# Kernel optimization log

Hardware: AMD Instinct MI355X
Metric: run time of the kernel (lower is better)

## Reference

```python
import jax, jax.numpy as jnp
import numpy as np

N_EMBD = 2048
N_HEAD = 8          # config.n_head // 2
HEAD_DIM = 256      # n_embd // (n_head // 2)
HALF = HEAD_DIM // 2
LAMBDA_INIT = 0.8
RMS_EPS = 1.1920929e-07  # torch float32 finfo eps (F.rms_norm default)


def _rms_norm(x):
    # F.rms_norm with no weight: x / sqrt(mean(x^2) + eps)
    return x * jax.lax.rsqrt(jnp.mean(x * x, axis=-1, keepdims=True) + RMS_EPS)


def setup_inputs() -> dict:
    key = jax.random.key(0)
    ks = jax.random.split(key, 10)
    B, T, C = 2, 2048, N_EMBD
    x = jax.random.normal(ks[0], (B, T, C), dtype=jnp.float32)
    wq = jax.random.normal(ks[1], (C, C), dtype=jnp.float32) * 0.02
    wk = jax.random.normal(ks[2], (C, C), dtype=jnp.float32) * 0.02
    wv = jax.random.normal(ks[3], (C, C), dtype=jnp.float32) * 0.02
    wo = jax.random.normal(ks[4], (C, C), dtype=jnp.float32) * 0.02
    lq1 = jax.random.normal(ks[5], (HEAD_DIM,), dtype=jnp.float32) * 0.1
    lk1 = jax.random.normal(ks[6], (HEAD_DIM,), dtype=jnp.float32) * 0.1
    lq2 = jax.random.normal(ks[7], (HEAD_DIM,), dtype=jnp.float32) * 0.1
    lk2 = jax.random.normal(ks[8], (HEAD_DIM,), dtype=jnp.float32) * 0.1
    return {"x": x, "wq": wq, "wk": wk, "wv": wv, "wo": wo,
            "lq1": lq1, "lk1": lk1, "lq2": lq2, "lk2": lk2}


def _causal_attn(q, k, v, mask):
    # q,k: [B,H,T,half], v: [B,H,T,HEAD_DIM]
    scale = 1.0 / jnp.sqrt(jnp.asarray(q.shape[-1], q.dtype))
    scores = jnp.einsum('bhqd,bhkd->bhqk', q, k) * scale
    scores = jnp.where(mask, scores, -jnp.inf)
    attn = jax.nn.softmax(scores, axis=-1)
    return jnp.einsum('bhqk,bhkd->bhqd', attn, v)


def reference(x, wq, wk, wv, wo, lq1, lk1, lq2, lk2):
    B, T, C = x.shape
    lambda_1 = jnp.exp(jnp.sum(lq1 * lk1))
    lambda_2 = jnp.exp(jnp.sum(lq2 * lk2))
    lambda_full = lambda_1 - lambda_2 + LAMBDA_INIT

    q = (x @ wq.T).reshape(B, T, N_HEAD, 2, HALF).transpose(0, 2, 1, 3, 4)  # [B,H,T,2,half]
    k = (x @ wk.T).reshape(B, T, N_HEAD, 2, HALF).transpose(0, 2, 1, 3, 4)
    v = (x @ wv.T).reshape(B, T, N_HEAD, HEAD_DIM).transpose(0, 2, 1, 3)    # [B,H,T,hd]

    q1 = _rms_norm(q[..., 0, :]); q2 = _rms_norm(q[..., 1, :])
    k1 = _rms_norm(k[..., 0, :]); k2 = _rms_norm(k[..., 1, :])

    mask = jnp.tril(jnp.ones((T, T), dtype=bool))
    y1 = _causal_attn(q1, k1, v, mask)
    y2 = _causal_attn(q2, k2, v, mask)
    y = y1 - lambda_full * y2                                               # [B,H,T,hd]

    y = y.transpose(0, 2, 1, 3).reshape(B, T, C)
    return (y @ wo.T) * (1.0 - LAMBDA_INIT)
```

## Files before the change

### kernel.cpp

```cpp
#include <hip/hip_runtime.h>
#include <stdint.h>


typedef __bf16 bf16;
typedef bf16 bf16x8 __attribute__((ext_vector_type(8)));
typedef bf16 bf16x4 __attribute__((ext_vector_type(4)));
typedef bf16 bf16x2 __attribute__((ext_vector_type(2)));
typedef float f32x4 __attribute__((ext_vector_type(4)));

typedef void __attribute__((address_space(1)))* gas_t;
typedef void __attribute__((address_space(3)))* las_t;

__device__ __forceinline__ void gload16(const void* g, void* l) {
  __builtin_amdgcn_global_load_lds((gas_t)(uintptr_t)g, (las_t)(uint32_t)(uintptr_t)l, 16, 0, 0);
}

__device__ __forceinline__ f32x4 mfma16x16(bf16x8 a, bf16x8 b, f32x4 c) {
  return __builtin_amdgcn_mfma_f32_16x16x32_bf16(a, b, c, 0, 0, 0);
}

__global__ __launch_bounds__(256) void cast_f32_bf16(const float* __restrict__ in,
                                                     bf16* __restrict__ out, int n4) {
  int i = blockIdx.x * 256 + threadIdx.x;
  if (i >= n4) return;
  float4 v = ((const float4*)in)[i];
  bf16x4 o;
  o[0] = (bf16)v.x; o[1] = (bf16)v.y; o[2] = (bf16)v.z; o[3] = (bf16)v.w;
  ((bf16x4*)out)[i] = o;
}

__global__ __launch_bounds__(256) void cast4_w(const float* __restrict__ a, const float* __restrict__ b,
                                               const float* __restrict__ c, const float* __restrict__ d,
                                               bf16* __restrict__ oa, bf16* __restrict__ ob,
                                               bf16* __restrict__ oc, bf16* __restrict__ od) {
  int w = blockIdx.y;
  const float* in = (w == 0) ? a : (w == 1) ? b : (w == 2) ? c : d;
  bf16* out = (w == 0) ? oa : (w == 1) ? ob : (w == 2) ? oc : od;
  int i = blockIdx.x * 256 + threadIdx.x;
  float4 v = ((const float4*)in)[i];
  bf16x4 o;
  o[0] = (bf16)v.x; o[1] = (bf16)v.y; o[2] = (bf16)v.z; o[3] = (bf16)v.w;
  ((bf16x4*)out)[i] = o;
}

__global__ void lambda_kernel(const float* __restrict__ lq1, const float* __restrict__ lk1,
                              const float* __restrict__ lq2, const float* __restrict__ lk2,
                              float* __restrict__ out) {
  __shared__ float red[8];
  int tid = threadIdx.x;
  float a = lq1[tid] * lk1[tid];
  float b = lq2[tid] * lk2[tid];
#pragma unroll
  for (int m = 32; m >= 1; m >>= 1) {
    a += __shfl_xor(a, m, 64);
    b += __shfl_xor(b, m, 64);
  }
  if ((tid & 63) == 0) { red[tid >> 6] = a; red[4 + (tid >> 6)] = b; }
  __syncthreads();
  if (tid == 0) {
    float s1 = red[0] + red[1] + red[2] + red[3];
    float s2 = red[4] + red[5] + red[6] + red[7];
    out[0] = expf(s1) - expf(s2) + 0.8f;
  }
}

__global__ __launch_bounds__(512, 2) void gemm_qkv8(const bf16* __restrict__ A,
                                                    const bf16* __restrict__ Bq,
                                                    const bf16* __restrict__ Bk,
                                                    const bf16* __restrict__ Bv,
                                                    bf16* __restrict__ Cq, bf16* __restrict__ Ck,
                                                    bf16* __restrict__ Cv) {
  __shared__ char lds[98304];
  const int K = 2048, nt = 64;

  int p = blockIdx.y * gridDim.x + blockIdx.x;
  int lid = (p & 7) * 48 + (p >> 3);
  const int bm = (lid / 24) * 256;
  const int bnG = (lid % 24) * 256;
  const int z = bnG >> 11;
  const int bn = bnG & 2047;
  const bf16* B = (z == 0) ? Bq : ((z == 1) ? Bk : Bv);

  const int tid = threadIdx.x;
  const int wid = tid >> 6, lane = tid & 63;
  const int l15 = lane & 15, lhi = lane >> 4;
  const int wm = wid >> 2, wn = wid & 3;

  const bf16* aS0 = A + (size_t)(bm + wid * 16 + l15) * K + lhi * 8;
  const bf16* bS0 = B + (size_t)(bn + wid * 16 + l15) * K + lhi * 8;

  auto stA = [&](int t, int pb) {
    char* d = lds + pb * 32768 + wid * 1024;
    const bf16* s = aS0 + t * 32;
    gload16(s, d);
    gload16(s + (size_t)128 * K, d + 8192);
  };
  auto stB = [&](int t, int pb) {
    char* d = lds + pb * 32768 + 16384 + wid * 1024;
    const bf16* s = bS0 + t * 32;
    gload16(s, d);
    gload16(s + (size_t)128 * K, d + 8192);
  };

  const f32x4 fz = {0.f, 0.f, 0.f, 0.f};
  f32x4 acc[8][4];
#pragma unroll
  for (int m = 0; m < 8; ++m)
#pragma unroll
    for (int n = 0; n < 4; ++n) acc[m][n] = fz;

  stA(0, 0); stB(0, 0);
  stA(1, 1); stB(1, 1);
  asm volatile("s_waitcnt vmcnt(4)" ::: "memory");
  __builtin_amdgcn_s_barrier();

  int cur = 0;
  for (int t = 0; t < nt; ++t) {
    const char* ab = lds + cur * 32768;
    const char* bb = ab + 16384;
    int nx2 = cur + 2; if (nx2 >= 3) nx2 -= 3;
    bf16x8 a[8], b0, b1;

#pragma unroll
    for (int m = 0; m < 8; ++m) a[m] = *(const bf16x8*)(ab + (wm * 8 + m) * 1024 + lane * 16);
    b0 = *(const bf16x8*)(bb + (wn * 4 + 0) * 1024 + lane * 16);
    b1 = *(const bf16x8*)(bb + (wn * 4 + 1) * 1024 + lane * 16);
    if (t + 2 < nt) stA(t + 2, nx2);
    __builtin_amdgcn_s_barrier();
    __builtin_amdgcn_s_setprio(1);
#pragma unroll
    for (int m = 0; m < 8; ++m) {
      acc[m][0] = mfma16x16(a[m], b0, acc[m][0]);
      acc[m][1] = mfma16x16(a[m], b1, acc[m][1]);
    }
    __builtin_amdgcn_s_setprio(0);
    __builtin_amdgcn_s_barrier();

    b0 = *(const bf16x8*)(bb + (wn * 4 + 2) * 1024 + lane * 16);
    b1 = *(const bf16x8*)(bb + (wn * 4 + 3) * 1024 + lane * 16);
    if (t + 2 < nt) stB(t + 2, nx2);
    __builtin_amdgcn_s_barrier();
    __builtin_amdgcn_s_setprio(1);
#pragma unroll
    for (int m = 0; m < 8; ++m) {
      acc[m][2] = mfma16x16(a[m], b0, acc[m][2]);
      acc[m][3] = mfma16x16(a[m], b1, acc[m][3]);
    }
    __builtin_amdgcn_s_setprio(0);
    if (t + 2 < nt) {
      asm volatile("s_waitcnt vmcnt(4)" ::: "memory");
    } else {
      asm volatile("s_waitcnt vmcnt(0)" ::: "memory");
    }
    __builtin_amdgcn_s_barrier();

    cur = (cur == 2) ? 0 : cur + 1;
  }

  if (z == 2) {
#pragma unroll
    for (int m = 0; m < 8; ++m)
#pragma unroll
      for (int n = 0; n < 4; ++n)
#pragma unroll
        for (int r = 0; r < 4; ++r) {
          int row = bm + wm * 128 + m * 16 + lhi * 4 + r;
          int col = bn + wn * 64 + n * 16 + l15;
          int bb3 = row >> 11, tt = row & 2047;
          Cv[(size_t)bb3 * 2048 * 2048 + (size_t)col * 2048 + tt] = (bf16)acc[m][n][r];
        }
    return;
  }
  float* ldsf = (float*)lds;
#pragma unroll
  for (int m = 0; m < 8; ++m)
#pragma unroll
    for (int r = 0; r < 4; ++r) {
      float s = acc[m][0][r] * acc[m][0][r] + acc[m][1][r] * acc[m][1][r] +
                acc[m][2][r] * acc[m][2][r] + acc[m][3][r] * acc[m][3][r];
      s += __shfl_xor(s, 1, 64);
      s += __shfl_xor(s, 2, 64);
      s += __shfl_xor(s, 4, 64);
      s += __shfl_xor(s, 8, 64);
      if (l15 == 0) ldsf[(wm * 128 + m * 16 + lhi * 4 + r) * 4 + wn] = s;
    }
  __syncthreads();
  const float osc = (z == 0) ? 0.08838834764831845f : 1.0f;
  bf16* C = (z == 0) ? Cq : Ck;
#pragma unroll
  for (int m = 0; m < 8; ++m) {
#pragma unroll
    for (int r = 0; r < 4; ++r) {
      int rl = wm * 128 + m * 16 + lhi * 4 + r;
      float tot = ldsf[rl * 4 + (wn & 2)] + ldsf[rl * 4 + (wn & 2) + 1];
      float sc = rsqrtf(tot * (1.0f / 128.0f) + 1.1920929e-07f) * osc;
#pragma unroll
      for (int n = 0; n < 4; ++n) {
        int col = bn + wn * 64 + n * 16 + l15;
        C[(size_t)(bm + rl) * 2048 + col] = (bf16)(acc[m][n][r] * sc);
      }
    }
  }
}

__global__ __launch_bounds__(256, 2) void gemm_out(const bf16* __restrict__ A, const bf16* __restrict__ B,
                                                   float* __restrict__ Cf) {
  __shared__ char lds[73728];
  const int K = 2048, nt = 64;

  int p = blockIdx.y * gridDim.x + blockIdx.x;
  int lid = (p & 7) * 32 + (p >> 3);
  const int bm = (lid / 16) * 256;
  const int bn = (lid % 16) * 128;

  const int tid = threadIdx.x;
  const int wid = tid >> 6, lane = tid & 63;
  const int l15 = lane & 15, lhi = lane >> 4;
  const int wm = wid >> 1, wn = wid & 1;

  const bf16* aB = A + (size_t)(bm + l15) * K + lhi * 8;
  const bf16* bB = B + (size_t)(bn + l15) * K + lhi * 8;

  auto stage = [&](int t, int pb) {
    char* base = lds + pb * 24576;
    const int k0 = t * 32;
    gload16(aB + (size_t)((0 + wid) * 16) * K + k0, base + wid * 1024);
    gload16(aB + (size_t)((4 + wid) * 16) * K + k0, base + 4096 + wid * 1024);
    gload16(aB + (size_t)((8 + wid) * 16) * K + k0, base + 8192 + wid * 1024);
    gload16(aB + (size_t)((12 + wid) * 16) * K + k0, base + 12288 + wid * 1024);
    gload16(bB + (size_t)((0 + wid) * 16) * K + k0, base + 16384 + wid * 1024);
    gload16(bB + (size_t)((4 + wid) * 16) * K + k0, base + 20480 + wid * 1024);
  };

  const f32x4 fz = {0.f, 0.f, 0.f, 0.f};
  f32x4 acc[8][4];
#pragma unroll
  for (int m = 0; m < 8; ++m)
#pragma unroll
    for (int n = 0; n < 4; ++n) acc[m][n] = fz;

  stage(0, 0);
  stage(1, 1);
  asm volatile("s_waitcnt vmcnt(6)" ::: "memory");
  __builtin_amdgcn_s_barrier();

  for (int t = 0; t < nt; ++t) {
    const char* ab = lds + (t % 3) * 24576;
    if (t + 2 < nt) stage(t + 2, (t + 2) % 3);
    bf16x8 a[8], b[4];
#pragma unroll
    for (int m = 0; m < 8; ++m)
      a[m] = *(const bf16x8*)(ab + (wm * 8 + m) * 1024 + lane * 16);
#pragma unroll
    for (int n = 0; n < 4; ++n)
      b[n] = *(const bf16x8*)(ab + 16384 + (wn * 4 + n) * 1024 + lane * 16);
    __builtin_amdgcn_s_setprio(1);
#pragma unroll
    for (int m = 0; m < 8; ++m)
#pragma unroll
      for (int n = 0; n < 4; ++n) acc[m][n] = mfma16x16(a[m], b[n], acc[m][n]);
    __builtin_amdgcn_s_setprio(0);
    if (t + 2 < nt) {
      asm volatile("s_waitcnt vmcnt(6)" ::: "memory");
    } else {
      asm volatile("s_waitcnt vmcnt(0)" ::: "memory");
    }
    __builtin_amdgcn_s_barrier();
  }

#pragma unroll
  for (int m = 0; m < 8; ++m)
#pragma unroll
    for (int n = 0; n < 4; ++n)
#pragma unroll
      for (int r = 0; r < 4; ++r) {
        int row = bm + wm * 128 + m * 16 + lhi * 4 + r;
        int col = bn + wn * 64 + n * 16 + l15;
        Cf[(size_t)row * 2048 + col] = acc[m][n][r] * 0.2f;
      }
}

__global__ __launch_bounds__(256) void attn_kernel(const bf16* __restrict__ qb, const bf16* __restrict__ kb,
                                                   const bf16* __restrict__ vtb, bf16* __restrict__ yb,
                                                   const float* __restrict__ lamp) {
  __shared__ char lds[57344];
  const int tid = threadIdx.x;
  const int wid = tid >> 6, lane = tid & 63;
  const int l15 = lane & 15, lhi = lane >> 4;
  char* vtl = lds + 32768;
  char* p1l = lds + 49152 + wid * 2048;
  char* p2l = p1l + 1024;
  const int qt = 31 - blockIdx.y;
  const int bh = blockIdx.x;
  const int b = bh >> 3, h = bh & 7;
  const int qr0 = qt * 64 + wid * 16;
  const float lam = lamp[0];

  const bf16* qrow = qb + (size_t)(b * 2048 + qr0 + l15) * 2048 + h * 256 + lhi * 8;
  bf16x8 q1f[4], q2f[4];
#pragma unroll
  for (int s = 0; s < 4; ++s) {
    q1f[s] = *(const bf16x8*)(qrow + s * 32);
    q2f[s] = *(const bf16x8*)(qrow + 128 + s * 32);
  }

  const f32x4 fz = {0.f, 0.f, 0.f, 0.f};
  f32x4 y1[16], y2[16];
#pragma unroll
  for (int f = 0; f < 16; ++f) { y1[f] = fz; y2[f] = fz; }
  float l1[4] = {0.f, 0.f, 0.f, 0.f}, l2[4] = {0.f, 0.f, 0.f, 0.f};

  const int nkt = 2 * qt + 2;
  const bf16* kbase = kb + (size_t)(b * 2048) * 2048 + h * 256;
  const bf16* vbase = vtb + (size_t)b * 2048 * 2048 + (size_t)(h * 256) * 2048;

  auto stageK = [&](int kt2, int p) {
    const int t0 = kt2 * 32;
    char* kd = lds + p * 16384 + wid * 1024;
    const bf16* sp = kbase + (size_t)(t0 + l15) * 2048 + wid * 32 + lhi * 8;
    gload16(sp, kd);
    gload16(sp + 16 * 2048, kd + 4096);
    gload16(sp + 128, kd + 8192);
    gload16(sp + 16 * 2048 + 128, kd + 12288);
  };
  auto stageVT = [&](int kt2) {
    const int t0 = kt2 * 32;
    const bf16* vp = vbase + (size_t)(wid * 16 + l15) * 2048 + t0 + lhi * 8;
#pragma unroll
    for (int i = 0; i < 4; ++i)
      gload16(vp + (size_t)i * 64 * 2048, vtl + (i * 4 + wid) * 1024);
  };

  stageK(0, 0);
  stageVT(0);
  __syncthreads();

  for (int kt = 0; kt < nkt; ++kt) {
    const int cur = kt & 1;
    const int t0 = kt * 32;
    const bool active = (t0 <= qr0 + 15);
    if (active) {
      const char* kc = lds + cur * 16384;
      f32x4 s1g[2], s2g[2];
#pragma unroll
      for (int g = 0; g < 2; ++g) {
        f32x4 a1 = fz, a2 = fz;
#pragma unroll
        for (int s = 0; s < 4; ++s) {
          a1 = mfma16x16(q1f[s], *(const bf16x8*)(kc + ((g * 4 + s) * 64 + lane) * 16), a1);
          a2 = mfma16x16(q2f[s], *(const bf16x8*)(kc + 8192 + ((g * 4 + s) * 64 + lane) * 16), a2);
        }
        s1g[g] = a1;
        s2g[g] = a2;
      }
      if (t0 + 31 > qr0) {
#pragma unroll
        for (int g = 0; g < 2; ++g) {
          int col = t0 + g * 16 + l15;
#pragma unroll
          for (int r = 0; r < 4; ++r) {
            int row = qr0 + lhi * 4 + r;
            if (col > row) { s1g[g][r] = -1e30f; s2g[g][r] = -1e30f; }
          }
        }
      }
#pragma unroll
      for (int g = 0; g < 2; ++g) {
#pragma unroll
        for (int r = 0; r < 4; ++r) {
          float p1 = __expf(s1g[g][r] - 12.0f);
          float p2 = __expf(s2g[g][r] - 12.0f);
          l1[r] += p1;
          l2[r] += p2;
          int off = ((lhi * 4 + r) * 32 + g * 16 + l15) * 2;
          *(bf16*)(p1l + off) = (bf16)p1;
          *(bf16*)(p2l + off) = (bf16)p2;
        }
      }
    }
    __syncthreads();
    if (active) {
      bf16x8 pa1 = *(const bf16x8*)(p1l + (l15 * 32 + lhi * 8) * 2);
      bf16x8 pa2 = *(const bf16x8*)(p2l + (l15 * 32 + lhi * 8) * 2);
#pragma unroll
      for (int f = 0; f < 16; ++f) {
        bf16x8 vf = *(const bf16x8*)(vtl + (f * 64 + lane) * 16);
        y1[f] = mfma16x16(pa1, vf, y1[f]);
        y2[f] = mfma16x16(pa2, vf, y2[f]);
      }
    }
    __syncthreads();
    if (kt + 1 < nkt) {
      stageK(kt + 1, cur ^ 1);
      stageVT(kt + 1);
    }
  }

#pragma unroll
  for (int r = 0; r < 4; ++r) {
    float s1 = l1[r], s2 = l2[r];
#pragma unroll
    for (int m = 1; m <= 8; m <<= 1) {
      s1 += __shfl_xor(s1, m, 64);
      s2 += __shfl_xor(s2, m, 64);
    }
    float inv1 = 1.f / s1;
    float inv2 = lam / s2;
    int row = qr0 + lhi * 4 + r;
    bf16* orow = yb + (size_t)(b * 2048 + row) * 2048 + h * 256 + l15;
#pragma unroll
    for (int f = 0; f < 16; ++f) {
      float v = y1[f][r] * inv1 - y2[f][r] * inv2;
      orow[f * 16] = (bf16)v;
    }
  }
}

extern "C" void kernel_launch(void* const* d_in, const int* in_sizes, int n_in,
                              void* d_out, int out_size, void* d_ws, size_t ws_size,
                              hipStream_t stream) {
  const float* x = (const float*)d_in[0];
  const float* wq = (const float*)d_in[1];
  const float* wk = (const float*)d_in[2];
  const float* wv = (const float*)d_in[3];
  const float* wo = (const float*)d_in[4];
  const float* lq1 = (const float*)d_in[5];
  const float* lk1 = (const float*)d_in[6];
  const float* lq2 = (const float*)d_in[7];
  const float* lk2 = (const float*)d_in[8];
  float* out = (float*)d_out;
  char* ws = (char*)d_ws;

  if (ws_size < 117440516) return;

  bf16* xb = (bf16*)(ws + 0);
  bf16* wqb = (bf16*)(ws + 16777216);
  bf16* wkb = (bf16*)(ws + 25165824);
  bf16* wvb = (bf16*)(ws + 33554432);
  bf16* wob = (bf16*)(ws + 41943040);
  bf16* qbuf = (bf16*)(ws + 50331648);
  bf16* kbuf = (bf16*)(ws + 67108864);
  bf16* vtb = (bf16*)(ws + 83886080);
  bf16* ybuf = (bf16*)(ws + 100663296);
  float* lam = (float*)(ws + 117440512);

  cast_f32_bf16<<<8192, 256, 0, stream>>>(x, xb, 2097152);
  cast4_w<<<dim3(4096, 4), 256, 0, stream>>>(wq, wk, wv, wo, wqb, wkb, wvb, wob);
  lambda_kernel<<<1, 256, 0, stream>>>(lq1, lk1, lq2, lk2, lam);

  gemm_qkv8<<<dim3(24, 16), 512, 0, stream>>>(xb, wqb, wkb, wvb, qbuf, kbuf, vtb);

  attn_kernel<<<dim3(16, 32), 256, 0, stream>>>(qbuf, kbuf, vtb, ybuf, lam);

  gemm_out<<<dim3(8, 32), 256, 0, stream>>>(ybuf, wob, out);
}
```

Before: 357.8 us.

## Prefetch attention K/V tiles through registers and reorder the attention grid

Replaces the double-buffered global_load_lds staging of K and V^T with register prefetch. The next tile's global loads are issued at the top of each iteration and written to a single LDS buffer after a barrier. This shrinks LDS from 56KB to 40KB, which may raise occupancy. The barrier between the softmax-probability store and the PV MFMAs is removed, since each wave only reads its own P region. MFMA sections are wrapped in s_setprio, and the 2D grid is flattened so heavy query tiles are scheduled first. The cost is an extra barrier per iteration and more VGPRs for the prefetch registers.

```diff
diff --git a/kernel.cpp b/kernel.cpp
--- a/kernel.cpp
+++ b/kernel.cpp
@@ -283,15 +283,18 @@
 __global__ __launch_bounds__(256) void attn_kernel(const bf16* __restrict__ qb, const bf16* __restrict__ kb,
                                                    const bf16* __restrict__ vtb, bf16* __restrict__ yb,
                                                    const float* __restrict__ lamp) {
-  __shared__ char lds[57344];
+  __shared__ char lds[40960];
   const int tid = threadIdx.x;
   const int wid = tid >> 6, lane = tid & 63;
   const int l15 = lane & 15, lhi = lane >> 4;
-  char* vtl = lds + 32768;
-  char* p1l = lds + 49152 + wid * 2048;
+  char* ktl = lds;
+  char* vtl = lds + 16384;
+  char* p1l = lds + 32768 + wid * 2048;
   char* p2l = p1l + 1024;
-  const int qt = 31 - blockIdx.y;
-  const int bh = blockIdx.x;
+
+  const int p = blockIdx.x;
+  const int bh = p & 15;
+  const int qt = (p < 256) ? (31 - (p >> 4)) : ((p - 256) >> 4);
   const int b = bh >> 3, h = bh & 7;
   const int qr0 = qt * 64 + wid * 16;
   const float lam = lamp[0];
@@ -314,45 +317,60 @@
   const bf16* kbase = kb + (size_t)(b * 2048) * 2048 + h * 256;
   const bf16* vbase = vtb + (size_t)b * 2048 * 2048 + (size_t)(h * 256) * 2048;
 
-  auto stageK = [&](int kt2, int p) {
-    const int t0 = kt2 * 32;
-    char* kd = lds + p * 16384 + wid * 1024;
-    const bf16* sp = kbase + (size_t)(t0 + l15) * 2048 + wid * 32 + lhi * 8;
-    gload16(sp, kd);
-    gload16(sp + 16 * 2048, kd + 4096);
-    gload16(sp + 128, kd + 8192);
-    gload16(sp + 16 * 2048 + 128, kd + 12288);
+  const bf16* kS = kbase + (size_t)l15 * 2048 + wid * 32 + lhi * 8;
+  const bf16* vS = vbase + (size_t)(wid * 16 + l15) * 2048 + lhi * 8;
+
+  int4 rk0, rk1, rk2, rk3, rv0, rv1, rv2, rv3;
+  auto loadRegs = [&](int kt2) {
+    const bf16* ks = kS + (size_t)(kt2 * 32) * 2048;
+    rk0 = *(const int4*)(ks);
+    rk1 = *(const int4*)(ks + (size_t)16 * 2048);
+    rk2 = *(const int4*)(ks + 128);
+    rk3 = *(const int4*)(ks + (size_t)16 * 2048 + 128);
+    const bf16* vs = vS + kt2 * 32;
+    rv0 = *(const int4*)(vs);
+    rv1 = *(const int4*)(vs + (size_t)64 * 2048);
+    rv2 = *(const int4*)(vs + (size_t)128 * 2048);
+    rv3 = *(const int4*)(vs + (size_t)192 * 2048);
   };
-  auto stageVT = [&](int kt2) {
-    const int t0 = kt2 * 32;
-    const bf16* vp = vbase + (size_t)(wid * 16 + l15) * 2048 + t0 + lhi * 8;
-#pragma unroll
-    for (int i = 0; i < 4; ++i)
-      gload16(vp + (size_t)i * 64 * 2048, vtl + (i * 4 + wid) * 1024);
+  auto writeLds = [&]() {
+    char* kd = ktl + wid * 1024 + lane * 16;
+    *(int4*)(kd) = rk0;
+    *(int4*)(kd + 4096) = rk1;
+    *(int4*)(kd + 8192) = rk2;
+    *(int4*)(kd + 12288) = rk3;
+    char* vd = vtl + wid * 1024 + lane * 16;
+    *(int4*)(vd) = rv0;
+    *(int4*)(vd + 4096) = rv1;
+    *(int4*)(vd + 8192) = rv2;
+    *(int4*)(vd + 12288) = rv3;
   };
 
-  stageK(0, 0);
-  stageVT(0);
+  loadRegs(0);
+  writeLds();
   __syncthreads();
 
   for (int kt = 0; kt < nkt; ++kt) {
-    const int cur = kt & 1;
     const int t0 = kt * 32;
     const bool active = (t0 <= qr0 + 15);
+    const bool hasNext = (kt + 1 < nkt);
+    if (hasNext) loadRegs(kt + 1);
+
     if (active) {
-      const char* kc = lds + cur * 16384;
       f32x4 s1g[2], s2g[2];
+      __builtin_amdgcn_s_setprio(1);
 #pragma unroll
       for (int g = 0; g < 2; ++g) {
         f32x4 a1 = fz, a2 = fz;
 #pragma unroll
         for (int s = 0; s < 4; ++s) {
-          a1 = mfma16x16(q1f[s], *(const bf16x8*)(kc + ((g * 4 + s) * 64 + lane) * 16), a1);
-          a2 = mfma16x16(q2f[s], *(const bf16x8*)(kc + 8192 + ((g * 4 + s) * 64 + lane) * 16), a2);
+          a1 = mfma16x16(q1f[s], *(const bf16x8*)(ktl + ((g * 4 + s) * 64 + lane) * 16), a1);
+          a2 = mfma16x16(q2f[s], *(const bf16x8*)(ktl + 8192 + ((g * 4 + s) * 64 + lane) * 16), a2);
         }
         s1g[g] = a1;
         s2g[g] = a2;
       }
+      __builtin_amdgcn_s_setprio(0);
       if (t0 + 31 > qr0) {
 #pragma unroll
         for (int g = 0; g < 2; ++g) {
@@ -377,23 +395,20 @@
           *(bf16*)(p2l + off) = (bf16)p2;
         }
       }
-    }
-    __syncthreads();
-    if (active) {
       bf16x8 pa1 = *(const bf16x8*)(p1l + (l15 * 32 + lhi * 8) * 2);
       bf16x8 pa2 = *(const bf16x8*)(p2l + (l15 * 32 + lhi * 8) * 2);
+      __builtin_amdgcn_s_setprio(1);
 #pragma unroll
       for (int f = 0; f < 16; ++f) {
         bf16x8 vf = *(const bf16x8*)(vtl + (f * 64 + lane) * 16);
         y1[f] = mfma16x16(pa1, vf, y1[f]);
         y2[f] = mfma16x16(pa2, vf, y2[f]);
       }
+      __builtin_amdgcn_s_setprio(0);
     }
     __syncthreads();
-    if (kt + 1 < nkt) {
-      stageK(kt + 1, cur ^ 1);
-      stageVT(kt + 1);
-    }
+    if (hasNext) writeLds();
+    __syncthreads();
   }
 
 #pragma unroll
@@ -450,7 +465,7 @@
 
   gemm_qkv8<<<dim3(24, 16), 512, 0, stream>>>(xb, wqb, wkb, wvb, qbuf, kbuf, vtb);
 
-  attn_kernel<<<dim3(16, 32), 256, 0, stream>>>(qbuf, kbuf, vtb, ybuf, lam);
+  attn_kernel<<<512, 256, 0, stream>>>(qbuf, kbuf, vtb, ybuf, lam);
 
   gemm_out<<<dim3(8, 32), 256, 0, stream>>>(ybuf, wob, out);
 }
```

Measured after the change: 403.4 us. +12.7%, slower.

## Double-buffer V tiles and prefetch next K/V before compute in attention

Applied to the files above, without the earlier changes.

The attention kernel now double-buffers the transposed V tile alongside K. It issues the global-to-LDS loads for the next K/V tile at the start of each iteration rather than after compute, so the loads overlap with the QK and PV MFMA work. The barrier between the P stores and the PV stage is dropped because each wave only reads its own P scratch. MFMA sections are wrapped in s_setprio, and the 2D grid is flattened with an explicit block-to-(bh, q-tile) mapping. The cost is more LDS (72KB), which may limit how many blocks fit on a CU.

```diff
diff --git a/kernel.cpp b/kernel.cpp
--- a/kernel.cpp
+++ b/kernel.cpp
@@ -283,15 +283,16 @@
 __global__ __launch_bounds__(256) void attn_kernel(const bf16* __restrict__ qb, const bf16* __restrict__ kb,
                                                    const bf16* __restrict__ vtb, bf16* __restrict__ yb,
                                                    const float* __restrict__ lamp) {
-  __shared__ char lds[57344];
+  __shared__ char lds[73728];
   const int tid = threadIdx.x;
   const int wid = tid >> 6, lane = tid & 63;
   const int l15 = lane & 15, lhi = lane >> 4;
-  char* vtl = lds + 32768;
-  char* p1l = lds + 49152 + wid * 2048;
+  char* p1l = lds + 65536 + wid * 2048;
   char* p2l = p1l + 1024;
-  const int qt = 31 - blockIdx.y;
-  const int bh = blockIdx.x;
+
+  const int p = blockIdx.x;
+  const int bh = p & 15;
+  const int qt = (p < 256) ? (31 - (p >> 4)) : ((p - 256) >> 4);
   const int b = bh >> 3, h = bh & 7;
   const int qr0 = qt * 64 + wid * 16;
   const float lam = lamp[0];
@@ -314,34 +315,41 @@
   const bf16* kbase = kb + (size_t)(b * 2048) * 2048 + h * 256;
   const bf16* vbase = vtb + (size_t)b * 2048 * 2048 + (size_t)(h * 256) * 2048;
 
-  auto stageK = [&](int kt2, int p) {
+  auto stageK = [&](int kt2, int pp) {
     const int t0 = kt2 * 32;
-    char* kd = lds + p * 16384 + wid * 1024;
+    char* kd = lds + pp * 16384 + wid * 1024;
     const bf16* sp = kbase + (size_t)(t0 + l15) * 2048 + wid * 32 + lhi * 8;
     gload16(sp, kd);
     gload16(sp + 16 * 2048, kd + 4096);
     gload16(sp + 128, kd + 8192);
     gload16(sp + 16 * 2048 + 128, kd + 12288);
   };
-  auto stageVT = [&](int kt2) {
+  auto stageVT = [&](int kt2, int pp) {
     const int t0 = kt2 * 32;
+    char* vd = lds + 32768 + pp * 16384;
     const bf16* vp = vbase + (size_t)(wid * 16 + l15) * 2048 + t0 + lhi * 8;
 #pragma unroll
     for (int i = 0; i < 4; ++i)
-      gload16(vp + (size_t)i * 64 * 2048, vtl + (i * 4 + wid) * 1024);
+      gload16(vp + (size_t)i * 64 * 2048, vd + (i * 4 + wid) * 1024);
   };
 
   stageK(0, 0);
-  stageVT(0);
+  stageVT(0, 0);
   __syncthreads();
 
   for (int kt = 0; kt < nkt; ++kt) {
     const int cur = kt & 1;
     const int t0 = kt * 32;
     const bool active = (t0 <= qr0 + 15);
+    if (kt + 1 < nkt) {
+      stageK(kt + 1, cur ^ 1);
+      stageVT(kt + 1, cur ^ 1);
+    }
     if (active) {
       const char* kc = lds + cur * 16384;
+      const char* vc = lds + 32768 + cur * 16384;
       f32x4 s1g[2], s2g[2];
+      __builtin_amdgcn_s_setprio(1);
 #pragma unroll
       for (int g = 0; g < 2; ++g) {
         f32x4 a1 = fz, a2 = fz;
@@ -353,6 +361,7 @@
         s1g[g] = a1;
         s2g[g] = a2;
       }
+      __builtin_amdgcn_s_setprio(0);
       if (t0 + 31 > qr0) {
 #pragma unroll
         for (int g = 0; g < 2; ++g) {
@@ -377,23 +386,18 @@
           *(bf16*)(p2l + off) = (bf16)p2;
         }
       }
-    }
-    __syncthreads();
-    if (active) {
       bf16x8 pa1 = *(const bf16x8*)(p1l + (l15 * 32 + lhi * 8) * 2);
       bf16x8 pa2 = *(const bf16x8*)(p2l + (l15 * 32 + lhi * 8) * 2);
+      __builtin_amdgcn_s_setprio(1);
 #pragma unroll
       for (int f = 0; f < 16; ++f) {
-        bf16x8 vf = *(const bf16x8*)(vtl + (f * 64 + lane) * 16);
+        bf16x8 vf = *(const bf16x8*)(vc + (f * 64 + lane) * 16);
         y1[f] = mfma16x16(pa1, vf, y1[f]);
         y2[f] = mfma16x16(pa2, vf, y2[f]);
       }
+      __builtin_amdgcn_s_setprio(0);
     }
     __syncthreads();
-    if (kt + 1 < nkt) {
-      stageK(kt + 1, cur ^ 1);
-      stageVT(kt + 1);
-    }
   }
 
 #pragma unroll
@@ -450,7 +454,7 @@
 
   gemm_qkv8<<<dim3(24, 16), 512, 0, stream>>>(xb, wqb, wkb, wvb, qbuf, kbuf, vtb);
 
-  attn_kernel<<<dim3(16, 32), 256, 0, stream>>>(qbuf, kbuf, vtb, ybuf, lam);
+  attn_kernel<<<512, 256, 0, stream>>>(qbuf, kbuf, vtb, ybuf, lam);
 
   gemm_out<<<dim3(8, 32), 256, 0, stream>>>(ybuf, wob, out);
 }
```

Result: faster. 346.6 us (-3.1%).
